# Kernel tuning notes

Measured on AMD Instinct MI355X. Metric: run time of the kernel, lower is better.

Reference implementation:

```python
import jax, jax.numpy as jnp
import numpy as np

B, N, C, K = 4, 4096, 64, 16
EPS = 1e-5


def _bn(x, g, b, m, v):
    # eval-mode BatchNorm2d on [B, C, N, K]
    scale = (g / jnp.sqrt(v + EPS))[None, :, None, None]
    return (x - m[None, :, None, None]) * scale + b[None, :, None, None]


def setup_inputs() -> dict:
    key = jax.random.key(0)
    ks = jax.random.split(key, 32)
    s = 0.05
    inp = {
        "p": jax.random.normal(ks[0], (B, N, 3), jnp.float32),
        "x": jax.random.normal(ks[1], (B, C, N), jnp.float32),
        "mask": jnp.ones((B, N), dtype=bool),
        # q/k/v 1x1 Conv1d weights [out, in] + bias
        "Wq": jax.random.normal(ks[2], (C, C)) * s, "bq": jax.random.normal(ks[3], (C,)) * s,
        "Wk": jax.random.normal(ks[4], (C, C)) * s, "bk": jax.random.normal(ks[5], (C,)) * s,
        "Wv": jax.random.normal(ks[6], (C, C)) * s, "bv": jax.random.normal(ks[7], (C,)) * s,
        # pos-enc: Conv2d(3->C, no bias), BN, ReLU, Conv2d(C->C)
        "pe_w1": jax.random.normal(ks[8], (C, 3)) * s,
        "pe_bn_g": jax.random.normal(ks[9], (C,)) * s + 1.0,
        "pe_bn_b": jax.random.normal(ks[10], (C,)) * s,
        "pe_bn_m": jax.random.normal(ks[11], (C,)) * s,
        "pe_bn_v": jax.random.uniform(ks[12], (C,), minval=0.5, maxval=1.5),
        "pe_w2": jax.random.normal(ks[13], (C, C)) * s, "pe_b2": jax.random.normal(ks[14], (C,)) * s,
        # attn: BN, ReLU, Conv2d(C->C, no bias), BN, ReLU, Conv2d(C->C)
        "at_bn0_g": jax.random.normal(ks[15], (C,)) * s + 1.0,
        "at_bn0_b": jax.random.normal(ks[16], (C,)) * s,
        "at_bn0_m": jax.random.normal(ks[17], (C,)) * s,
        "at_bn0_v": jax.random.uniform(ks[18], (C,), minval=0.5, maxval=1.5),
        "at_w1": jax.random.normal(ks[19], (C, C)) * s,
        "at_bn1_g": jax.random.normal(ks[20], (C,)) * s + 1.0,
        "at_bn1_b": jax.random.normal(ks[21], (C,)) * s,
        "at_bn1_m": jax.random.normal(ks[22], (C,)) * s,
        "at_bn1_v": jax.random.uniform(ks[23], (C,), minval=0.5, maxval=1.5),
        "at_w2": jax.random.normal(ks[24], (C, C)) * s, "at_b2": jax.random.normal(ks[25], (C,)) * s,
    }
    return inp


def reference(p, x, mask, Wq, bq, Wk, bk, Wv, bv,
              pe_w1, pe_bn_g, pe_bn_b, pe_bn_m, pe_bn_v, pe_w2, pe_b2,
              at_bn0_g, at_bn0_b, at_bn0_m, at_bn0_v, at_w1,
              at_bn1_g, at_bn1_b, at_bn1_m, at_bn1_v, at_w2, at_b2):
    # q, k, v: 1x1 Conv1d -> [B, C, N]
    q = jnp.einsum('oc,bcn->bon', Wq, x) + bq[None, :, None]
    k = jnp.einsum('oc,bcn->bon', Wk, x) + bk[None, :, None]
    v = jnp.einsum('oc,bcn->bon', Wv, x) + bv[None, :, None]

    # ---- knn_point(K, p, p): Euclidean cdist, zero-point masking, topk smallest
    sq = jnp.sum(p * p, axis=-1)                                   # [B, N]
    d2 = sq[:, :, None] + sq[:, None, :] - 2.0 * jnp.einsum('bnc,bmc->bnm', p, p)
    dist = jnp.sqrt(jnp.maximum(d2, 0.0))                          # [B, N, N]
    valid = ~jnp.all(p == 0, axis=-1)                              # [B, N]
    dist = jnp.where(valid[:, None, :], dist, jnp.inf)
    _, idx = jax.lax.top_k(-dist, K)                               # [B, N, K]

    gather = jax.vmap(lambda a, i: a[i])                           # ([N,C],[N,K]) -> [N,K,C]
    n_k = gather(jnp.transpose(k, (0, 2, 1)), idx)                 # [B, N, K, C]
    n_v = gather(jnp.transpose(v, (0, 2, 1)), idx)                 # [B, N, K, C]
    n_p = gather(p, idx)                                           # [B, N, K, 3]

    rel = p[:, :, None, :] - n_p                                   # [B, N, K, 3]
    rel = jnp.transpose(rel, (0, 3, 1, 2))                         # [B, 3, N, K]

    # position encoding MLP
    h = jnp.einsum('oc,bcnk->bonk', pe_w1, rel)
    h = jax.nn.relu(_bn(h, pe_bn_g, pe_bn_b, pe_bn_m, pe_bn_v))
    n_r = jnp.einsum('oc,bcnk->bonk', pe_w2, h) + pe_b2[None, :, None, None]  # [B,C,N,K]

    # attention MLP on (q - n_k + n_r)
    a = q[:, :, :, None] - jnp.transpose(n_k, (0, 3, 1, 2)) + n_r
    a = jax.nn.relu(_bn(a, at_bn0_g, at_bn0_b, at_bn0_m, at_bn0_v))
    a = jnp.einsum('oc,bcnk->bonk', at_w1, a)
    a = jax.nn.relu(_bn(a, at_bn1_g, at_bn1_b, at_bn1_m, at_bn1_v))
    a = jnp.einsum('oc,bcnk->bonk', at_w2, a) + at_b2[None, :, None, None]

    # mask [B,N] broadcast to [B,C,N,K] (masks query rows, as in original)
    a = jnp.where(mask[:, None, :, None], a, -1e10)
    a = jax.nn.softmax(a, axis=-1)
    a = jnp.where(jnp.isnan(a), 0.0, a)

    y = jnp.sum(a * (jnp.transpose(n_v, (0, 3, 1, 2)) + n_r), axis=-1)  # [B, C, N]
    return (p, y)
```

## Files before the change

kernel.cpp:

```cpp
#include <hip/hip_runtime.h>
#include <stdint.h>

#define NB 4
#define NP 4096
#define NC 64
#define NK 16
#define BN_EPS 1e-5f

typedef __attribute__((ext_vector_type(8))) short short8;
typedef __attribute__((ext_vector_type(4))) float f32x4;
typedef unsigned long long u64;

__device__ __forceinline__ short f2bf(float f) {
    unsigned u = __float_as_uint(f);
    unsigned r = (u + 0x7FFFu + ((u >> 16) & 1u)) >> 16;
    return (short)(unsigned short)r;
}

__global__ __launch_bounds__(256) void px_kernel(const float* __restrict__ p,
                                                 float4* __restrict__ px,
                                                 float* __restrict__ pcopy) {
    int gid = blockIdx.x * 256 + threadIdx.x;
    float x = p[gid * 3 + 0], y = p[gid * 3 + 1], z = p[gid * 3 + 2];
    pcopy[gid * 3 + 0] = x; pcopy[gid * 3 + 1] = y; pcopy[gid * 3 + 2] = z;
    float sq = fmaf(z, z, fmaf(y, y, x * x));
    bool inv = (x == 0.0f) && (y == 0.0f) && (z == 0.0f);
    px[gid] = make_float4(x, y, z, inv ? __builtin_inff() : sq);
}

__global__ __launch_bounds__(128) void qkv_kernel(
        const float* __restrict__ x,
        const float* __restrict__ Wq, const float* __restrict__ bq,
        const float* __restrict__ Wk, const float* __restrict__ bk,
        const float* __restrict__ Wv, const float* __restrict__ bv,
        float* __restrict__ outbase) {
    __shared__ float wt[NC * NC];
    __shared__ float bsh[NC];
    const int which = blockIdx.y;
    const float* W    = which == 0 ? Wq : which == 1 ? Wk : Wv;
    const float* bias = which == 0 ? bq : which == 1 ? bk : bv;
    float* out = outbase + (size_t)which * NB * NP * NC;

    for (int e = threadIdx.x; e < NC * NC; e += 128)
        wt[(e & 63) * NC + (e >> 6)] = W[e];
    if (threadIdx.x < NC) bsh[threadIdx.x] = bias[threadIdx.x];
    __syncthreads();

    const int gid = blockIdx.x * 128 + threadIdx.x;
    const int b = gid >> 12, n = gid & (NP - 1);

    float acc[NC];
#pragma unroll
    for (int o = 0; o < NC; ++o) acc[o] = bsh[o];

    const float* xp = x + (size_t)b * NC * NP + n;
    for (int c = 0; c < NC; ++c) {
        float xc = xp[(size_t)c * NP];
        const float4* wr = (const float4*)&wt[c * NC];
#pragma unroll
        for (int o4 = 0; o4 < NC / 4; ++o4) {
            float4 w4 = wr[o4];
            acc[o4 * 4 + 0] = fmaf(w4.x, xc, acc[o4 * 4 + 0]);
            acc[o4 * 4 + 1] = fmaf(w4.y, xc, acc[o4 * 4 + 1]);
            acc[o4 * 4 + 2] = fmaf(w4.z, xc, acc[o4 * 4 + 2]);
            acc[o4 * 4 + 3] = fmaf(w4.w, xc, acc[o4 * 4 + 3]);
        }
    }
    float4* op = (float4*)(out + (size_t)gid * NC);
#pragma unroll
    for (int o4 = 0; o4 < NC / 4; ++o4)
        op[o4] = make_float4(acc[o4 * 4 + 0], acc[o4 * 4 + 1],
                             acc[o4 * 4 + 2], acc[o4 * 4 + 3]);
}

#define KQW 4
#define KCAP 64

__global__ __launch_bounds__(256) void knn_kernel(const float4* __restrict__ px,
                                                  int* __restrict__ idxout) {
    __shared__ float tb[4][KQW * 64];
    __shared__ u64 sbuf[16][KCAP];
    __shared__ int scnt[16];
    const int l = threadIdx.x & 63;
    const int w = threadIdx.x >> 6;
    const int gw = blockIdx.x * 4 + w;
    const int q0 = gw * KQW;
    const int b  = q0 >> 12;
    const float4* pb = px + (size_t)b * NP;

    float4 pn[KQW];
#pragma unroll
    for (int j = 0; j < KQW; ++j) pn[j] = px[q0 + j];
    if (l < KQW) scnt[w * KQW + l] = 0;
    __builtin_amdgcn_wave_barrier();

    float k1[KQW];
#pragma unroll
    for (int j = 0; j < KQW; ++j) k1[j] = __builtin_inff();
#pragma unroll 4
    for (int i = 0; i < NP / 64; ++i) {
        float4 pm = pb[i * 64 + l];
#pragma unroll
        for (int j = 0; j < KQW; ++j) {
            float dot = fmaf(pm.z, pn[j].z, fmaf(pm.y, pn[j].y, pm.x * pn[j].x));
            float d2 = fmaxf((pn[j].w + pm.w) - 2.0f * dot, 0.0f);
            k1[j] = fminf(k1[j], d2);
        }
    }
#pragma unroll
    for (int j = 0; j < KQW; ++j) tb[w][j * 64 + l] = k1[j];
    __builtin_amdgcn_wave_barrier();

    float T[KQW];
#pragma unroll
    for (int j = 0; j < KQW; ++j) {
        const float* tj = &tb[w][j * 64];
        int rank = 0;
#pragma unroll 4
        for (int t = 0; t < 64; t += 4) {
            f32x4 v = *(const f32x4*)&tj[t];
            rank += (v[0] < k1[j]) + (v[1] < k1[j]) + (v[2] < k1[j]) + (v[3] < k1[j]);
        }
        float cand = (rank <= 15) ? k1[j] : -__builtin_inff();
#pragma unroll
        for (int off = 32; off; off >>= 1)
            cand = fmaxf(cand, __shfl_xor(cand, off));
        T[j] = cand;
    }

#pragma unroll 2
    for (int i = 0; i < NP / 64; ++i) {
        int m = i * 64 + l;
        float4 pm = pb[m];
#pragma unroll
        for (int j = 0; j < KQW; ++j) {
            float dot = fmaf(pm.z, pn[j].z, fmaf(pm.y, pn[j].y, pm.x * pn[j].x));
            float d2 = fmaxf((pn[j].w + pm.w) - 2.0f * dot, 0.0f);
            if (d2 <= T[j]) {
                int pos = atomicAdd(&scnt[w * KQW + j], 1);
                if (pos < KCAP)
                    sbuf[w * KQW + j][pos] =
                        ((u64)__float_as_uint(d2) << 32) | (unsigned int)m;
            }
        }
    }
    __builtin_amdgcn_wave_barrier();

#pragma unroll 1
    for (int j = 0; j < KQW; ++j) {
        int cnt = scnt[w * KQW + j];
        if (cnt > KCAP) cnt = KCAP;
        if (l < cnt) {
            const u64* sb = sbuf[w * KQW + j];
            u64 kj = sb[l];
            int rank = 0;
            for (int t = 0; t < cnt; ++t) rank += (sb[t] < kj);
            if (rank < NK)
                idxout[(size_t)(q0 + j) * NK + rank] = (int)(kj & 0xffffffffu);
        }
    }
}

#define QPW 4
#define HBSTR 72
#define DBSTR 20

__device__ __forceinline__ short8 pack8(float4 a, float4 b) {
    short8 r;
    r[0] = f2bf(a.x); r[1] = f2bf(a.y); r[2] = f2bf(a.z); r[3] = f2bf(a.w);
    r[4] = f2bf(b.x); r[5] = f2bf(b.y); r[6] = f2bf(b.z); r[7] = f2bf(b.w);
    return r;
}

__device__ __forceinline__ void gemm_stage(const short8* wf ,
                                           const unsigned short* HBw,
                                           float* DBw, int tok, int quad) {
    short8 b0 = *(const short8*)((const char*)HBw + tok * (HBSTR * 2) + quad * 16);
    short8 b1 = *(const short8*)((const char*)HBw + tok * (HBSTR * 2) + 64 + quad * 16);
#pragma unroll
    for (int ob = 0; ob < 4; ++ob) {
        f32x4 acc = {0.0f, 0.0f, 0.0f, 0.0f};
        acc = __builtin_amdgcn_mfma_f32_16x16x32_bf16(wf[ob * 2 + 0], b0, acc, 0, 0, 0);
        acc = __builtin_amdgcn_mfma_f32_16x16x32_bf16(wf[ob * 2 + 1], b1, acc, 0, 0, 0);
#pragma unroll
        for (int r = 0; r < 4; ++r)
            DBw[(ob * 16 + quad * 4 + r) * DBSTR + tok] = acc[r];
    }
}

__global__ __launch_bounds__(256, 2) void fused_mfma_kernel(
        const float4* __restrict__ px, const int* __restrict__ idx,
        const float* __restrict__ qT, const float* __restrict__ kT,
        const float* __restrict__ vT,
        const float* __restrict__ pe_w1,
        const float* __restrict__ pe_g, const float* __restrict__ pe_b,
        const float* __restrict__ pe_m, const float* __restrict__ pe_v,
        const float* __restrict__ pe_w2, const float* __restrict__ pe_b2,
        const float* __restrict__ b0g, const float* __restrict__ b0b,
        const float* __restrict__ b0m, const float* __restrict__ b0v,
        const float* __restrict__ at_w1,
        const float* __restrict__ b1g, const float* __restrict__ b1b,
        const float* __restrict__ b1m, const float* __restrict__ b1v,
        const float* __restrict__ at_w2, const float* __restrict__ at_b2,
        float* __restrict__ yout) {
    __shared__ __align__(16) unsigned short HB[4][16 * HBSTR];
    __shared__ __align__(16) float DB[4][64 * DBSTR];
    __shared__ __align__(16) int IB[4][NK];

    const int l    = threadIdx.x & 63;
    const int w    = threadIdx.x >> 6;
    const int c    = l;
    const int tok  = l & 15;
    const int quad = l >> 4;

    short8 wf[3][8];
    {
        const float* Ws[3] = {pe_w2, at_w1, at_w2};
#pragma unroll
        for (int mat = 0; mat < 3; ++mat)
#pragma unroll
            for (int ob = 0; ob < 4; ++ob)
#pragma unroll
                for (int ch = 0; ch < 2; ++ch) {
                    const float* src = Ws[mat] + (ob * 16 + tok) * NC + ch * 32 + quad * 8;
                    float4 a = *(const float4*)src;
                    float4 bq4 = *(const float4*)(src + 4);
                    wf[mat][ob * 2 + ch] = pack8(a, bq4);
                }
    }

    const float pw0 = pe_w1[c * 3 + 0], pw1 = pe_w1[c * 3 + 1], pw2v = pe_w1[c * 3 + 2];
    const float pes = pe_g[c] / sqrtf(pe_v[c] + BN_EPS);
    const float peb = fmaf(-pe_m[c], pes, pe_b[c]);
    const float s0  = b0g[c] / sqrtf(b0v[c] + BN_EPS);
    const float bb0 = fmaf(-b0m[c], s0, b0b[c]);
    const float s1  = b1g[c] / sqrtf(b1v[c] + BN_EPS);
    const float bb1 = fmaf(-b1m[c], s1, b1b[c]);
    const float peb2 = pe_b2[c];
    const float ab2  = at_b2[c];

    unsigned short* HBw = HB[w];
    float* DBw = DB[w];
    int* IBw = IB[w];

    const int gw = blockIdx.x * 4 + w;

    for (int jq = 0; jq < QPW; ++jq) {
        const int qi = gw * QPW + jq;
        const int b = qi >> 12, n = qi & (NP - 1);
        const float4 pn = px[qi];
        const float qv = qT[(size_t)qi * NC + c];

        if (l < NK) IBw[l] = idx[qi * NK + l];
        __builtin_amdgcn_wave_barrier();

        int mreg[NK];
#pragma unroll
        for (int g = 0; g < 4; ++g) {
            int4 m4 = *(const int4*)&IBw[g * 4];
            mreg[g * 4 + 0] = m4.x; mreg[g * 4 + 1] = m4.y;
            mreg[g * 4 + 2] = m4.z; mreg[g * 4 + 3] = m4.w;
        }

        float4 pmr[NK];
#pragma unroll
        for (int k = 0; k < NK; ++k) pmr[k] = px[b * NP + mreg[k]];

#pragma unroll
        for (int k = 0; k < NK; ++k) {
            float r0 = pn.x - pmr[k].x, r1 = pn.y - pmr[k].y, r2 = pn.z - pmr[k].z;
            float h = fmaf(pw2v, r2, fmaf(pw1, r1, pw0 * r0));
            h = fmaxf(fmaf(h, pes, peb), 0.0f);
            HBw[k * HBSTR + c] = (unsigned short)f2bf(h);
        }
        __builtin_amdgcn_wave_barrier();

        float kreg[NK];
#pragma unroll
        for (int k = 0; k < NK; ++k)
            kreg[k] = kT[((size_t)(b * NP + mreg[k])) * NC + c];

        gemm_stage(wf[0], HBw, DBw, tok, quad);
        __builtin_amdgcn_wave_barrier();

        float nr[NK];
#pragma unroll
        for (int j = 0; j < 4; ++j) {
            f32x4 v4 = *(const f32x4*)(DBw + c * DBSTR + j * 4);
            nr[j * 4 + 0] = v4[0] + peb2;
            nr[j * 4 + 1] = v4[1] + peb2;
            nr[j * 4 + 2] = v4[2] + peb2;
            nr[j * 4 + 3] = v4[3] + peb2;
        }
        __builtin_amdgcn_wave_barrier();

#pragma unroll
        for (int k = 0; k < NK; ++k) {
            float a0 = qv - kreg[k] + nr[k];
            a0 = fmaxf(fmaf(a0, s0, bb0), 0.0f);
            HBw[k * HBSTR + c] = (unsigned short)f2bf(a0);
        }
        __builtin_amdgcn_wave_barrier();

        float vreg[NK];
#pragma unroll
        for (int k = 0; k < NK; ++k)
            vreg[k] = vT[((size_t)(b * NP + mreg[k])) * NC + c];

        gemm_stage(wf[1], HBw, DBw, tok, quad);
        __builtin_amdgcn_wave_barrier();

#pragma unroll
        for (int j = 0; j < 4; ++j) {
            f32x4 v4 = *(const f32x4*)(DBw + c * DBSTR + j * 4);
#pragma unroll
            for (int r = 0; r < 4; ++r) {
                float a2 = fmaxf(fmaf(v4[r], s1, bb1), 0.0f);
                HBw[(j * 4 + r) * HBSTR + c] = (unsigned short)f2bf(a2);
            }
        }
        __builtin_amdgcn_wave_barrier();

        gemm_stage(wf[2], HBw, DBw, tok, quad);
        __builtin_amdgcn_wave_barrier();

        float a3[NK];
#pragma unroll
        for (int j = 0; j < 4; ++j) {
            f32x4 v4 = *(const f32x4*)(DBw + c * DBSTR + j * 4);
            a3[j * 4 + 0] = v4[0] + ab2;
            a3[j * 4 + 1] = v4[1] + ab2;
            a3[j * 4 + 2] = v4[2] + ab2;
            a3[j * 4 + 3] = v4[3] + ab2;
        }
        __builtin_amdgcn_wave_barrier();

        float mx = a3[0];
#pragma unroll
        for (int k = 1; k < NK; ++k) mx = fmaxf(mx, a3[k]);
        float ssum = 0.0f, yacc = 0.0f;
#pragma unroll
        for (int k = 0; k < NK; ++k) {
            float e = __expf(a3[k] - mx);
            ssum += e;
            yacc = fmaf(e, vreg[k] + nr[k], yacc);
        }
        yout[((size_t)(b * NC + c)) * NP + n] = yacc / ssum;
        __builtin_amdgcn_wave_barrier();
    }
}

extern "C" void kernel_launch(void* const* d_in, const int* in_sizes, int n_in,
                              void* d_out, int out_size, void* d_ws, size_t ws_size,
                              hipStream_t stream) {
    const float* p    = (const float*)d_in[0];
    const float* x    = (const float*)d_in[1];
    const float* Wq = (const float*)d_in[3];  const float* bq = (const float*)d_in[4];
    const float* Wk = (const float*)d_in[5];  const float* bk = (const float*)d_in[6];
    const float* Wv = (const float*)d_in[7];  const float* bv = (const float*)d_in[8];
    const float* pe_w1 = (const float*)d_in[9];
    const float* pe_g  = (const float*)d_in[10]; const float* pe_b = (const float*)d_in[11];
    const float* pe_m  = (const float*)d_in[12]; const float* pe_v = (const float*)d_in[13];
    const float* pe_w2 = (const float*)d_in[14]; const float* pe_b2 = (const float*)d_in[15];
    const float* b0g = (const float*)d_in[16]; const float* b0b = (const float*)d_in[17];
    const float* b0m = (const float*)d_in[18]; const float* b0v = (const float*)d_in[19];
    const float* at_w1 = (const float*)d_in[20];
    const float* b1g = (const float*)d_in[21]; const float* b1b = (const float*)d_in[22];
    const float* b1m = (const float*)d_in[23]; const float* b1v = (const float*)d_in[24];
    const float* at_w2 = (const float*)d_in[25]; const float* at_b2 = (const float*)d_in[26];

    const size_t BNC = (size_t)NB * NP * NC;
    float* ws  = (float*)d_ws;
    float* qT  = ws;
    float* kT  = qT + BNC;
    float* vT  = kT + BNC;
    float4* px = (float4*)(vT + BNC);
    int* idx   = (int*)(px + (size_t)NB * NP);

    float* outp = (float*)d_out;
    float* y = outp + (size_t)NB * NP * 3;

    px_kernel<<<dim3(64), dim3(256), 0, stream>>>(p, px, outp);
    qkv_kernel<<<dim3(128, 3), dim3(128), 0, stream>>>(x, Wq, bq, Wk, bk, Wv, bv, qT);
    knn_kernel<<<dim3(1024), dim3(256), 0, stream>>>(px, idx);
    fused_mfma_kernel<<<dim3(1024), dim3(256), 0, stream>>>(
        px, idx, qT, kT, vT, pe_w1, pe_g, pe_b, pe_m, pe_v, pe_w2, pe_b2,
        b0g, b0b, b0m, b0v, at_w1, b1g, b1b, b1m, b1v, at_w2, at_b2, y);
}
```

Baseline: 219.4 us.

## Move pe_w2 fragments to LDS, raise occupancy, prefetch next query indices

Keeps the first GEMM's weight fragments in shared memory instead of registers, freeing VGPRs so launch bounds can ask for 4 blocks per CU instead of 2. Neighbor indices, the query point and the q value are now loaded directly into registers and prefetched one query ahead, which removes the LDS staging of idx. The softmax reads the final GEMM output from LDS twice instead of holding it in registers. The trade-off is extra LDS reads per GEMM, and forcing 4 blocks per CU may cause register spills.

After: 272.6 us. 1.24x slower.

```diff
diff --git a/kernel.cpp b/kernel.cpp
--- a/kernel.cpp
+++ b/kernel.cpp
@@ -188,7 +188,25 @@
     }
 }
 
-__global__ __launch_bounds__(256, 2) void fused_mfma_kernel(
+__device__ __forceinline__ void gemm_stage_lds(const short8* __restrict__ WF, int l,
+                                               const unsigned short* HBw,
+                                               float* DBw, int tok, int quad) {
+    short8 b0 = *(const short8*)((const char*)HBw + tok * (HBSTR * 2) + quad * 16);
+    short8 b1 = *(const short8*)((const char*)HBw + tok * (HBSTR * 2) + 64 + quad * 16);
+#pragma unroll
+    for (int ob = 0; ob < 4; ++ob) {
+        f32x4 acc = {0.0f, 0.0f, 0.0f, 0.0f};
+        short8 a0 = WF[(ob * 2 + 0) * 64 + l];
+        short8 a1 = WF[(ob * 2 + 1) * 64 + l];
+        acc = __builtin_amdgcn_mfma_f32_16x16x32_bf16(a0, b0, acc, 0, 0, 0);
+        acc = __builtin_amdgcn_mfma_f32_16x16x32_bf16(a1, b1, acc, 0, 0, 0);
+#pragma unroll
+        for (int r = 0; r < 4; ++r)
+            DBw[(ob * 16 + quad * 4 + r) * DBSTR + tok] = acc[r];
+    }
+}
+
+__global__ __launch_bounds__(256, 4) void fused_mfma_kernel(
         const float4* __restrict__ px, const int* __restrict__ idx,
         const float* __restrict__ qT, const float* __restrict__ kT,
         const float* __restrict__ vT,
@@ -205,7 +223,7 @@
         float* __restrict__ yout) {
     __shared__ __align__(16) unsigned short HB[4][16 * HBSTR];
     __shared__ __align__(16) float DB[4][64 * DBSTR];
-    __shared__ __align__(16) int IB[4][NK];
+    __shared__ __align__(16) short8 WF0[8][64];
 
     const int l    = threadIdx.x & 63;
     const int w    = threadIdx.x >> 6;
@@ -213,11 +231,11 @@
     const int tok  = l & 15;
     const int quad = l >> 4;
 
-    short8 wf[3][8];
+    short8 wf[2][8];
     {
-        const float* Ws[3] = {pe_w2, at_w1, at_w2};
-#pragma unroll
-        for (int mat = 0; mat < 3; ++mat)
+        const float* Ws[2] = {at_w1, at_w2};
+#pragma unroll
+        for (int mat = 0; mat < 2; ++mat)
 #pragma unroll
             for (int ob = 0; ob < 4; ++ob)
 #pragma unroll
@@ -227,6 +245,17 @@
                     float4 bq4 = *(const float4*)(src + 4);
                     wf[mat][ob * 2 + ch] = pack8(a, bq4);
                 }
+    }
+    if (w == 0) {
+#pragma unroll
+        for (int ob = 0; ob < 4; ++ob)
+#pragma unroll
+            for (int ch = 0; ch < 2; ++ch) {
+                const float* src = pe_w2 + (ob * 16 + tok) * NC + ch * 32 + quad * 8;
+                float4 a = *(const float4*)src;
+                float4 bq4 = *(const float4*)(src + 4);
+                WF0[ob * 2 + ch][l] = pack8(a, bq4);
+            }
     }
 
     const float pw0 = pe_w1[c * 3 + 0], pw1 = pe_w1[c * 3 + 1], pw2v = pe_w1[c * 3 + 2];
@@ -239,32 +268,33 @@
     const float peb2 = pe_b2[c];
     const float ab2  = at_b2[c];
 
+    __syncthreads();
+
     unsigned short* HBw = HB[w];
     float* DBw = DB[w];
-    int* IBw = IB[w];
+    const short8* WFp = &WF0[0][0];
 
     const int gw = blockIdx.x * 4 + w;
+    const int q0 = gw * QPW;
+
+    const int4* ip = (const int4*)(idx + (size_t)q0 * NK);
+    int4 nid0 = ip[0], nid1 = ip[1], nid2 = ip[2], nid3 = ip[3];
+    float4 pn = px[q0];
+    float qv = qT[(size_t)q0 * NC + c];
 
     for (int jq = 0; jq < QPW; ++jq) {
-        const int qi = gw * QPW + jq;
+        const int qi = q0 + jq;
         const int b = qi >> 12, n = qi & (NP - 1);
-        const float4 pn = px[qi];
-        const float qv = qT[(size_t)qi * NC + c];
-
-        if (l < NK) IBw[l] = idx[qi * NK + l];
-        __builtin_amdgcn_wave_barrier();
-
-        int mreg[NK];
-#pragma unroll
-        for (int g = 0; g < 4; ++g) {
-            int4 m4 = *(const int4*)&IBw[g * 4];
-            mreg[g * 4 + 0] = m4.x; mreg[g * 4 + 1] = m4.y;
-            mreg[g * 4 + 2] = m4.z; mreg[g * 4 + 3] = m4.w;
-        }
-
+
+        int mreg[NK] = {nid0.x, nid0.y, nid0.z, nid0.w,
+                        nid1.x, nid1.y, nid1.z, nid1.w,
+                        nid2.x, nid2.y, nid2.z, nid2.w,
+                        nid3.x, nid3.y, nid3.z, nid3.w};
+
+        const float4* pxb = px + (size_t)b * NP;
         float4 pmr[NK];
 #pragma unroll
-        for (int k = 0; k < NK; ++k) pmr[k] = px[b * NP + mreg[k]];
+        for (int k = 0; k < NK; ++k) pmr[k] = pxb[mreg[k]];
 
 #pragma unroll
         for (int k = 0; k < NK; ++k) {
@@ -280,7 +310,7 @@
         for (int k = 0; k < NK; ++k)
             kreg[k] = kT[((size_t)(b * NP + mreg[k])) * NC + c];
 
-        gemm_stage(wf[0], HBw, DBw, tok, quad);
+        gemm_stage_lds(WFp, l, HBw, DBw, tok, quad);
         __builtin_amdgcn_wave_barrier();
 
         float nr[NK];
@@ -307,7 +337,14 @@
         for (int k = 0; k < NK; ++k)
             vreg[k] = vT[((size_t)(b * NP + mreg[k])) * NC + c];
 
-        gemm_stage(wf[1], HBw, DBw, tok, quad);
+        if (jq + 1 < QPW) {
+            const int4* ip2 = (const int4*)(idx + (size_t)(qi + 1) * NK);
+            nid0 = ip2[0]; nid1 = ip2[1]; nid2 = ip2[2]; nid3 = ip2[3];
+            pn = px[qi + 1];
+            qv = qT[(size_t)(qi + 1) * NC + c];
+        }
+
+        gemm_stage(wf[0], HBw, DBw, tok, quad);
         __builtin_amdgcn_wave_barrier();
 
 #pragma unroll
@@ -321,29 +358,27 @@
         }
         __builtin_amdgcn_wave_barrier();
 
-        gemm_stage(wf[2], HBw, DBw, tok, quad);
-        __builtin_amdgcn_wave_barrier();
-
-        float a3[NK];
+        gemm_stage(wf[1], HBw, DBw, tok, quad);
+        __builtin_amdgcn_wave_barrier();
+
+        float mxr = -__builtin_inff();
 #pragma unroll
         for (int j = 0; j < 4; ++j) {
             f32x4 v4 = *(const f32x4*)(DBw + c * DBSTR + j * 4);
-            a3[j * 4 + 0] = v4[0] + ab2;
-            a3[j * 4 + 1] = v4[1] + ab2;
-            a3[j * 4 + 2] = v4[2] + ab2;
-            a3[j * 4 + 3] = v4[3] + ab2;
-        }
-        __builtin_amdgcn_wave_barrier();
-
-        float mx = a3[0];
-#pragma unroll
-        for (int k = 1; k < NK; ++k) mx = fmaxf(mx, a3[k]);
+            mxr = fmaxf(mxr, fmaxf(fmaxf(v4[0], v4[1]), fmaxf(v4[2], v4[3])));
+        }
+        const float mx = mxr + ab2;
         float ssum = 0.0f, yacc = 0.0f;
 #pragma unroll
-        for (int k = 0; k < NK; ++k) {
-            float e = __expf(a3[k] - mx);
-            ssum += e;
-            yacc = fmaf(e, vreg[k] + nr[k], yacc);
+        for (int j = 0; j < 4; ++j) {
+            f32x4 v4 = *(const f32x4*)(DBw + c * DBSTR + j * 4);
+#pragma unroll
+            for (int r = 0; r < 4; ++r) {
+                const int k = j * 4 + r;
+                float e = __expf((v4[r] + ab2) - mx);
+                ssum += e;
+                yacc = fmaf(e, vreg[k] + nr[k], yacc);
+            }
         }
         yout[((size_t)(b * NC + c)) * NP + n] = yacc / ssum;
         __builtin_amdgcn_wave_barrier();
```
